# Kernel tuning notes

Measured on AMD Instinct MI355X. Metric: run time of the kernel, lower is better.

## Reference

```python
import jax, jax.numpy as jnp
import numpy as np

N = 100000      # nodes
E = 1600000     # edges (avg degree 16)
F = 64          # input node features
H = 128         # hidden channels
R = 20          # num relations (edge types)
G = 64          # graphs in batch
C = 10          # num classes
L = 2           # num RGCN layers
EPS = 1e-5      # BatchNorm eps


def setup_inputs() -> dict:
    key = jax.random.key(0)
    ks = jax.random.split(key, 14)
    s = 0.05
    return {
        "x": jax.random.normal(ks[0], (N, F), jnp.float32),
        "edge_index": jax.random.randint(ks[1], (2, E), 0, N, jnp.int32),
        "edge_type": jax.random.randint(ks[2], (E,), 0, R, jnp.int32),
        "batch": jnp.sort(jax.random.randint(ks[3], (N,), 0, G, jnp.int32)),
        # params
        "w_in": jax.random.normal(ks[4], (F, H), jnp.float32) * s,
        "b_in": jnp.zeros((H,), jnp.float32),
        "rel_w": jax.random.normal(ks[5], (L, R, H, H), jnp.float32) * s,
        "root_w": jax.random.normal(ks[6], (L, H, H), jnp.float32) * s,
        "conv_b": jnp.zeros((L, H), jnp.float32),
        "bn_g": jnp.ones((L, H), jnp.float32),
        "bn_b": jnp.zeros((L, H), jnp.float32),
        "w_out": jax.random.normal(ks[7], (H, C), jnp.float32) * s,
        "b_out": jnp.zeros((C,), jnp.float32),
    }


def reference(x, edge_index, edge_type, batch, w_in, b_in, rel_w, root_w,
              conv_b, bn_g, bn_b, w_out, b_out):
    # input MLP (dropout is identity in eval)
    h = jax.nn.relu(x @ w_in + b_in)

    src, dst = edge_index[0], edge_index[1]
    # per-(dst,relation) in-degree for RGCNConv mean aggregation
    comb = dst * R + edge_type                             # [E]
    cnt = jax.ops.segment_sum(jnp.ones((E,), jnp.float32), comb,
                              num_segments=N * R)
    edge_norm = (1.0 / jnp.maximum(cnt, 1.0))[comb]        # [E]

    for l in range(L):
        msg = h[src] * edge_norm[:, None]                  # [E, H] normalized source feats
        out = h @ root_w[l] + conv_b[l]                    # root/self transform + bias
        for r in range(R):
            mask = (edge_type == r).astype(h.dtype)        # [E]
            agg = jax.ops.segment_sum(msg * mask[:, None], dst,
                                      num_segments=N)      # [N, H] per-relation mean
            out = out + agg @ rel_w[l, r]
        # BatchNorm1d (training-mode batch statistics over nodes)
        mu = out.mean(axis=0)
        var = out.var(axis=0)
        out = (out - mu) * jax.lax.rsqrt(var + EPS) * bn_g[l] + bn_b[l]
        h = jax.nn.relu(out)                               # dropout = identity (eval)

    # global mean pool over graphs
    sums = jax.ops.segment_sum(h, batch, num_segments=G)   # [G, H]
    counts = jax.ops.segment_sum(jnp.ones((N,), h.dtype), batch, num_segments=G)
    pooled = sums / jnp.maximum(counts, 1.0)[:, None]

    logits = pooled @ w_out + b_out                        # [G, C]
    return jax.nn.sigmoid(logits)
```

## Files before the change

### kernel.cpp

```cpp
#include <hip/hip_runtime.h>

#define N_NODES 100000
#define E_EDGES 1600000
#define F_IN    64
#define H_DIM   128
#define R_REL   20
#define G_GRAPHS 64
#define C_CLASSES 10
#define L_LAYERS 2
#define BN_EPS  1e-5f
#define RN      (R_REL * N_NODES)

typedef unsigned short u16;
typedef unsigned int   u32;
typedef __attribute__((ext_vector_type(8))) short short8;
typedef __attribute__((ext_vector_type(4))) float f32x4;

static __device__ __forceinline__ float bf2f(u16 u) {
    u32 b = ((u32)u) << 16;
    return __builtin_bit_cast(float, b);
}
static __device__ __forceinline__ u16 f2bf(float f) {
    u32 x = __builtin_bit_cast(u32, f);
    u32 r = x + 0x7fff + ((x >> 16) & 1);
    return (u16)(r >> 16);
}


__global__ void count_kernel(const int* __restrict__ ei, const int* __restrict__ et,
                             int* __restrict__ hist) {
    for (int e = blockIdx.x * blockDim.x + threadIdx.x; e < E_EDGES;
         e += gridDim.x * blockDim.x) {
        int t = et[e];
        int d = ei[E_EDGES + e];
        atomicAdd(&hist[t * N_NODES + d], 1);
    }
}

__global__ void scan1_kernel(const int* __restrict__ in, int* __restrict__ out,
                             int* __restrict__ part, int n) {
    __shared__ int s[256];
    int t = threadIdx.x;
    int base = blockIdx.x * 1024;
    int v[4]; int sum = 0;
#pragma unroll
    for (int j = 0; j < 4; ++j) {
        int i = base + t * 4 + j;
        v[j] = (i < n) ? in[i] : 0;
        sum += v[j];
    }
    s[t] = sum;
    __syncthreads();
    for (int off = 1; off < 256; off <<= 1) {
        int x = (t >= off) ? s[t - off] : 0;
        __syncthreads();
        s[t] += x;
        __syncthreads();
    }
    if (t == 255) part[blockIdx.x] = s[255];
    int run = s[t] - sum;
#pragma unroll
    for (int j = 0; j < 4; ++j) {
        int i = base + t * 4 + j;
        if (i < n) out[i] = run;
        run += v[j];
    }
}

__global__ void scan2_kernel(int* __restrict__ part, int nb) {
    __shared__ int s[256];
    int t = threadIdx.x;
    int loc[8]; int sum = 0;
#pragma unroll
    for (int j = 0; j < 8; ++j) {
        int i = t * 8 + j;
        loc[j] = (i < nb) ? part[i] : 0;
        sum += loc[j];
    }
    s[t] = sum;
    __syncthreads();
    for (int off = 1; off < 256; off <<= 1) {
        int x = (t >= off) ? s[t - off] : 0;
        __syncthreads();
        s[t] += x;
        __syncthreads();
    }
    int run = s[t] - sum;
#pragma unroll
    for (int j = 0; j < 8; ++j) {
        int i = t * 8 + j;
        if (i < nb) part[i] = run;
        run += loc[j];
    }
}

__global__ void scan3_kernel(int* __restrict__ out, int* __restrict__ cur2,
                             const int* __restrict__ part, int n) {
    for (int i = blockIdx.x * blockDim.x + threadIdx.x; i < n;
         i += gridDim.x * blockDim.x) {
        int v = out[i] + part[i >> 10];
        out[i] = v;
        cur2[i] = v;
    }
}

__global__ void finalize_kernel(int* __restrict__ off2) {
    if (threadIdx.x == 0) off2[RN] = E_EDGES;
}

__global__ void bucket_kernel(const int* __restrict__ ei, const int* __restrict__ et,
                              int* __restrict__ cur2, int2* __restrict__ epair) {
    for (int e = blockIdx.x * blockDim.x + threadIdx.x; e < E_EDGES;
         e += gridDim.x * blockDim.x) {
        int t = et[e];
        int s = ei[e];
        int d = ei[E_EDGES + e];
        int pos = atomicAdd(&cur2[t * N_NODES + d], 1);
        epair[pos] = make_int2(s, d);
    }
}

template<int K>
__global__ void pack_w(const float* __restrict__ W, u16* __restrict__ Wp) {
    const float* w = W + (size_t)blockIdx.x * K * H_DIM;
    u16* p = Wp + (size_t)blockIdx.x * K * H_DIM;
    for (int o = threadIdx.x; o < K * H_DIM; o += blockDim.x) {
        int j  = o & 7;
        int l  = (o >> 3) & 63;
        int ct = (o >> 9) & 7;
        int kt = o >> 12;
        int k  = kt * 32 + (l >> 4) * 8 + j;
        int n  = ct * 16 + (l & 15);
        p[o] = f2bf(w[(size_t)k * H_DIM + n]);
    }
}

__global__ void cvt_bf16_kernel(const float* __restrict__ in, u16* __restrict__ out, int n4) {
    for (int i = blockIdx.x * blockDim.x + threadIdx.x; i < n4;
         i += gridDim.x * blockDim.x) {
        float4 v = ((const float4*)in)[i];
        ushort4 o;
        o.x = f2bf(v.x); o.y = f2bf(v.y); o.z = f2bf(v.z); o.w = f2bf(v.w);
        ((ushort4*)out)[i] = o;
    }
}

template<int K, bool RELU, bool HASBIAS, bool OUTBF16>
__global__ __launch_bounds__(256)
void mfma_dense(const u16* __restrict__ A, const u16* __restrict__ Wp,
                const float* __restrict__ bias, void* __restrict__ OutV, int M) {
    constexpr int CH = K / 8;
    __shared__ u16 Ws[K * H_DIM];
    __shared__ u16 As[64 * H_DIM];

    for (int o = threadIdx.x; o < K * H_DIM / 8; o += 256)
        ((short8*)Ws)[o] = ((const short8*)Wp)[o];

    const int lane = threadIdx.x & 63;
    const int wave = threadIdx.x >> 6;
    const int l15  = lane & 15;
    const int kgrp = lane >> 4;
    const int arow = wave * 16 + l15;

    for (int tb = blockIdx.x * 64; tb < M; tb += gridDim.x * 64) {
        __syncthreads();
        for (int o = threadIdx.x; o < 64 * CH; o += 256) {
            int row = o / CH, cc = o % CH;
            int grow = tb + row;
            short8 v = {0,0,0,0,0,0,0,0};
            if (grow < M) v = *(const short8*)&A[(size_t)grow * K + cc * 8];
            *(short8*)&As[row * K + ((cc ^ (row & 7)) * 8)] = v;
        }
        __syncthreads();

        f32x4 acc[8];
#pragma unroll
        for (int i = 0; i < 8; ++i) {
            acc[i][0] = 0.f; acc[i][1] = 0.f; acc[i][2] = 0.f; acc[i][3] = 0.f;
        }
#pragma unroll
        for (int kt = 0; kt < K / 32; ++kt) {
            short8 af = *(const short8*)&As[arow * K + (((kt * 4 + kgrp) ^ (arow & 7)) * 8)];
#pragma unroll
            for (int ct = 0; ct < 8; ++ct) {
                short8 bf = *(const short8*)&Ws[(((kt * 8 + ct) * 64) + lane) * 8];
                acc[ct] = __builtin_amdgcn_mfma_f32_16x16x32_bf16(af, bf, acc[ct], 0, 0, 0);
            }
        }

        if (OUTBF16) {
            __syncthreads();
#pragma unroll
            for (int ct = 0; ct < 8; ++ct) {
#pragma unroll
                for (int r = 0; r < 4; ++r) {
                    int row = wave * 16 + kgrp * 4 + r;
                    int col = ct * 16 + l15;
                    float v = acc[ct][r];
                    if (HASBIAS) v += bias[col];
                    if (RELU)    v = fmaxf(v, 0.f);
                    As[row * H_DIM + ((((col >> 3) ^ (row & 7)) << 3) | (col & 7))] = f2bf(v);
                }
            }
            __syncthreads();
            u16* Out = (u16*)OutV;
            for (int o = threadIdx.x; o < 64 * 16; o += 256) {
                int row = o >> 4, cc = o & 15;
                int grow = tb + row;
                if (grow < M)
                    *(short8*)&Out[(size_t)grow * H_DIM + cc * 8] =
                        *(const short8*)&As[row * H_DIM + ((cc ^ (row & 7)) << 3)];
            }
        } else {
            float* Out = (float*)OutV;
#pragma unroll
            for (int ct = 0; ct < 8; ++ct) {
#pragma unroll
                for (int r = 0; r < 4; ++r) {
                    int grow = tb + wave * 16 + kgrp * 4 + r;
                    if (grow < M) {
                        float v = acc[ct][r];
                        if (HASBIAS) v += bias[ct * 16 + l15];
                        if (RELU)    v = fmaxf(v, 0.f);
                        Out[(size_t)grow * H_DIM + ct * 16 + l15] = v;
                    }
                }
            }
        }
    }
}

__global__ __launch_bounds__(256, 4)
void rgcn_conv(const u16* __restrict__ h, const u16* __restrict__ Wrel,
               const u16* __restrict__ Wroot, const float* __restrict__ bias,
               const int2* __restrict__ epair, const int* __restrict__ off2,
               float* __restrict__ outb, float* __restrict__ bn_sums) {
    __shared__ int offs[R_REL][65];
    __shared__ u16 Abf[64 * H_DIM];
    __shared__ float bnS[H_DIM], bnSS[H_DIM];

    const int d0 = blockIdx.x * 64;
    for (int i = threadIdx.x; i < R_REL * 65; i += 256) {
        int r = i / 65, j = i % 65;
        offs[r][j] = off2[r * N_NODES + min(d0 + j, N_NODES)];
    }
    if (threadIdx.x < H_DIM) { bnS[threadIdx.x] = 0.f; bnSS[threadIdx.x] = 0.f; }

    const int lane = threadIdx.x & 63;
    const int wv   = threadIdx.x >> 6;
    const int l15  = lane & 15;
    const int kgrp = lane >> 4;
    const int arow = wv * 16 + l15;
    const u32* h2  = (const u32*)h;
    u32* Ab32 = (u32*)Abf;

    f32x4 acc[8];
#pragma unroll
    for (int i = 0; i < 8; ++i) {
        acc[i][0] = 0.f; acc[i][1] = 0.f; acc[i][2] = 0.f; acc[i][3] = 0.f;
    }

    auto flushrow = [&](int dcur, int cnt, float f0, float f1) {
        float nm = 1.0f / (float)cnt;
        int dr = dcur - d0;
        u32 pk = (u32)f2bf(f0 * nm) | ((u32)f2bf(f1 * nm) << 16);
        Ab32[dr * 64 + ((((lane >> 2) ^ (dr & 7)) << 2) | (lane & 3))] = pk;
    };

    __syncthreads();

    for (int r = 0; r < R_REL; ++r) {
        const int estart = __builtin_amdgcn_readfirstlane(offs[r][wv * 16]);
        const int eend   = __builtin_amdgcn_readfirstlane(offs[r][wv * 16 + 16]);
        if (eend <= estart) continue;

#pragma unroll
        for (int i = 0; i < 16; ++i)
            Ab32[(wv * 16 + i) * 64 + lane] = 0u;

        {
            const int last = eend - 1;
            int ss[16], dd[16];
            u32 rv[16];
#pragma unroll
            for (int j = 0; j < 16; ++j) {
                int2 pr = epair[min(estart + j, last)];
                ss[j] = pr.x; dd[j] = pr.y;
            }
#pragma unroll
            for (int j = 0; j < 16; ++j)
                rv[j] = h2[(size_t)ss[j] * 64 + lane];

            int dcur = -1, cnt = 0;
            float f0 = 0.f, f1 = 0.f;
#pragma unroll
            for (int j = 0; j < 16; ++j) {
                if (estart + j < eend) {
                    if (dd[j] != dcur) {
                        if (dcur >= 0) flushrow(dcur, cnt, f0, f1);
                        dcur = dd[j]; f0 = 0.f; f1 = 0.f; cnt = 0;
                    }
                    f0 += bf2f((u16)(rv[j] & 0xffff));
                    f1 += bf2f((u16)(rv[j] >> 16));
                    cnt++;
                }
            }
            for (int e = estart + 16; e < eend; e += 16) {
                int ss2[16], dd2[16];
                u32 rv2[16];
#pragma unroll
                for (int j = 0; j < 16; ++j) {
                    int2 pr = epair[min(e + j, last)];
                    ss2[j] = pr.x; dd2[j] = pr.y;
                }
#pragma unroll
                for (int j = 0; j < 16; ++j)
                    rv2[j] = h2[(size_t)ss2[j] * 64 + lane];
#pragma unroll
                for (int j = 0; j < 16; ++j) {
                    if (e + j < eend) {
                        if (dd2[j] != dcur) {
                            if (dcur >= 0) flushrow(dcur, cnt, f0, f1);
                            dcur = dd2[j]; f0 = 0.f; f1 = 0.f; cnt = 0;
                        }
                        f0 += bf2f((u16)(rv2[j] & 0xffff));
                        f1 += bf2f((u16)(rv2[j] >> 16));
                        cnt++;
                    }
                }
            }
            if (dcur >= 0) flushrow(dcur, cnt, f0, f1);
        }

        const u16* Wr = Wrel + (size_t)r * H_DIM * H_DIM;
#pragma unroll
        for (int kt = 0; kt < 4; ++kt) {
            short8 af = *(const short8*)&Abf[arow * H_DIM + (((kt * 4 + kgrp) ^ (arow & 7)) * 8)];
#pragma unroll
            for (int ct = 0; ct < 8; ++ct) {
                short8 bf = *(const short8*)&Wr[(((kt * 8 + ct) * 64) + lane) * 8];
                acc[ct] = __builtin_amdgcn_mfma_f32_16x16x32_bf16(af, bf, acc[ct], 0, 0, 0);
            }
        }
    }

    {
        const int hrow = min(d0 + arow, N_NODES - 1);
#pragma unroll
        for (int kt = 0; kt < 4; ++kt) {
            short8 af = *(const short8*)&h[(size_t)hrow * H_DIM + kt * 32 + kgrp * 8];
#pragma unroll
            for (int ct = 0; ct < 8; ++ct) {
                short8 bf = *(const short8*)&Wroot[(((kt * 8 + ct) * 64) + lane) * 8];
                acc[ct] = __builtin_amdgcn_mfma_f32_16x16x32_bf16(af, bf, acc[ct], 0, 0, 0);
            }
        }
    }

#pragma unroll
    for (int ct = 0; ct < 8; ++ct) {
        float bv = bias[ct * 16 + l15];
        float sl = 0.f, sq = 0.f;
#pragma unroll
        for (int rr = 0; rr < 4; ++rr) {
            int grow = d0 + wv * 16 + kgrp * 4 + rr;
            if (grow < N_NODES) {
                float v = acc[ct][rr] + bv;
                outb[(size_t)grow * H_DIM + ct * 16 + l15] = v;
                sl += v;
                sq += v * v;
            }
        }
        sl += __shfl_xor(sl, 16); sl += __shfl_xor(sl, 32);
        sq += __shfl_xor(sq, 16); sq += __shfl_xor(sq, 32);
        if (kgrp == 0) {
            atomicAdd(&bnS[ct * 16 + l15], sl);
            atomicAdd(&bnSS[ct * 16 + l15], sq);
        }
    }
    __syncthreads();
    if (threadIdx.x < H_DIM) {
        atomicAdd(&bn_sums[threadIdx.x], bnS[threadIdx.x]);
        atomicAdd(&bn_sums[H_DIM + threadIdx.x], bnSS[threadIdx.x]);
    }
}

__global__ void bn_apply(const float* __restrict__ X, const float* __restrict__ sums,
                         const float* __restrict__ gg, const float* __restrict__ bb,
                         u16* __restrict__ Hout) {
    __shared__ float sc[H_DIM], sh[H_DIM];
    if (threadIdx.x < H_DIM) {
        float mean = sums[threadIdx.x] * (1.0f / N_NODES);
        float var  = sums[H_DIM + threadIdx.x] * (1.0f / N_NODES) - mean * mean;
        float inv  = rsqrtf(var + BN_EPS) * gg[threadIdx.x];
        sc[threadIdx.x] = inv;
        sh[threadIdx.x] = bb[threadIdx.x] - mean * inv;
    }
    __syncthreads();
    int total = N_NODES * (H_DIM / 4);
    for (int idx = blockIdx.x * 256 + threadIdx.x; idx < total; idx += gridDim.x * 256) {
        float4 v = ((const float4*)X)[idx];
        int c = (idx & 31) << 2;
        ushort4 o;
        o.x = f2bf(fmaxf(v.x * sc[c + 0] + sh[c + 0], 0.f));
        o.y = f2bf(fmaxf(v.y * sc[c + 1] + sh[c + 1], 0.f));
        o.z = f2bf(fmaxf(v.z * sc[c + 2] + sh[c + 2], 0.f));
        o.w = f2bf(fmaxf(v.w * sc[c + 3] + sh[c + 3], 0.f));
        ((ushort4*)Hout)[idx] = o;
    }
}

__global__ void pool_kernel(const u16* __restrict__ Hf, const int* __restrict__ batch,
                            float* __restrict__ pool, float* __restrict__ pcnt) {
    int col  = threadIdx.x & 127;
    int half = threadIdx.x >> 7;
    int chunk = (N_NODES + gridDim.x - 1) / gridDim.x;
    int start = blockIdx.x * chunk;
    int end   = min(N_NODES, start + chunk);
    int curg = -1;
    float acc = 0.f, c = 0.f;
    for (int row = start + half; row < end; row += 2) {
        int g = batch[row];
        if (g != curg) {
            if (curg >= 0) {
                atomicAdd(&pool[curg * H_DIM + col], acc);
                if (col == 0) atomicAdd(&pcnt[curg], c);
            }
            curg = g; acc = 0.f; c = 0.f;
        }
        acc += bf2f(Hf[(size_t)row * H_DIM + col]);
        c += 1.f;
    }
    if (curg >= 0) {
        atomicAdd(&pool[curg * H_DIM + col], acc);
        if (col == 0) atomicAdd(&pcnt[curg], c);
    }
}

__global__ void logits_kernel(const float* __restrict__ pool, const float* __restrict__ pcnt,
                              const float* __restrict__ w_out, const float* __restrict__ b_out,
                              float* __restrict__ out) {
    int g = blockIdx.x;
    __shared__ float p[H_DIM];
    float cnt = fmaxf(pcnt[g], 1.0f);
    p[threadIdx.x] = pool[g * H_DIM + threadIdx.x] / cnt;
    __syncthreads();
    if (threadIdx.x < C_CLASSES) {
        float acc = b_out[threadIdx.x];
        for (int k = 0; k < H_DIM; ++k)
            acc += p[k] * w_out[k * C_CLASSES + threadIdx.x];
        out[g * C_CLASSES + threadIdx.x] = 1.0f / (1.0f + expf(-acc));
    }
}

static inline size_t align256(size_t x) { return (x + 255) & ~(size_t)255; }

extern "C" void kernel_launch(void* const* d_in, const int* in_sizes, int n_in,
                              void* d_out, int out_size, void* d_ws, size_t ws_size,
                              hipStream_t stream) {
    const float* x      = (const float*)d_in[0];
    const int*   ei     = (const int*)d_in[1];
    const int*   et     = (const int*)d_in[2];
    const int*   batch  = (const int*)d_in[3];
    const float* w_in   = (const float*)d_in[4];
    const float* b_in   = (const float*)d_in[5];
    const float* rel_w  = (const float*)d_in[6];
    const float* root_w = (const float*)d_in[7];
    const float* conv_b = (const float*)d_in[8];
    const float* bn_g   = (const float*)d_in[9];
    const float* bn_b   = (const float*)d_in[10];
    const float* w_out  = (const float*)d_in[11];
    const float* b_out  = (const float*)d_in[12];
    float* out = (float*)d_out;

    char* ws = (char*)d_ws;
    size_t off = 0;
    u16*   h_bf  = (u16*)(ws + off);  off += align256((size_t)N_NODES * H_DIM * 2);
    float* outb  = (float*)(ws + off); off += align256((size_t)N_NODES * H_DIM * 4);
    u16*   x_bf  = (u16*)(ws + off);  off += align256((size_t)N_NODES * F_IN * 2);
    int*   off2  = (int*)(ws + off);  off += align256((size_t)(RN + 1) * 4 + 256);
    int*   cur2  = (int*)(ws + off);  off += align256((size_t)RN * 4);
    int2*  e_pair = (int2*)(ws + off); off += align256((size_t)E_EDGES * 8 + 256);
    u16*   wp_in   = (u16*)(ws + off); off += align256((size_t)F_IN * H_DIM * 2);
    u16*   wp_root = (u16*)(ws + off); off += align256((size_t)L_LAYERS * H_DIM * H_DIM * 2);
    u16*   wp_rel  = (u16*)(ws + off); off += align256((size_t)L_LAYERS * R_REL * H_DIM * H_DIM * 2);
    int*   scan_part  = (int*)(ws + off); off += align256(2048 * 4);
    float* bn_sums    = (float*)(ws + off); off += align256(2 * H_DIM * 4);
    float* pool       = (float*)(ws + off); off += align256((size_t)G_GRAPHS * H_DIM * 4);
    float* pcnt       = (float*)(ws + off); off += 256;

    hipMemsetAsync(cur2, 0, (size_t)RN * 4, stream);
    count_kernel<<<1024, 256, 0, stream>>>(ei, et, cur2);
    const int NB = (RN + 1023) / 1024;
    scan1_kernel<<<NB, 256, 0, stream>>>(cur2, off2, scan_part, RN);
    scan2_kernel<<<1, 256, 0, stream>>>(scan_part, NB);
    scan3_kernel<<<2048, 256, 0, stream>>>(off2, cur2, scan_part, RN);
    finalize_kernel<<<1, 64, 0, stream>>>(off2);
    bucket_kernel<<<2048, 256, 0, stream>>>(ei, et, cur2, e_pair);

    cvt_bf16_kernel<<<2048, 256, 0, stream>>>(x, x_bf, N_NODES * F_IN / 4);
    pack_w<F_IN><<<1, 256, 0, stream>>>(w_in, wp_in);
    pack_w<H_DIM><<<L_LAYERS, 256, 0, stream>>>(root_w, wp_root);
    pack_w<H_DIM><<<L_LAYERS * R_REL, 256, 0, stream>>>(rel_w, wp_rel);

    mfma_dense<F_IN, true, true, true><<<dim3(640), 256, 0, stream>>>(
        x_bf, wp_in, b_in, h_bf, N_NODES);

    const int CONV_BLOCKS = (N_NODES + 63) / 64;
    for (int l = 0; l < L_LAYERS; ++l) {
        hipMemsetAsync(bn_sums, 0, 2 * H_DIM * 4, stream);
        rgcn_conv<<<dim3(CONV_BLOCKS), 256, 0, stream>>>(
            h_bf, wp_rel + (size_t)l * R_REL * H_DIM * H_DIM,
            wp_root + (size_t)l * H_DIM * H_DIM, conv_b + (size_t)l * H_DIM,
            e_pair, off2, outb, bn_sums);
        bn_apply<<<2048, 256, 0, stream>>>(outb, bn_sums,
                                           bn_g + (size_t)l * H_DIM,
                                           bn_b + (size_t)l * H_DIM, h_bf);
    }

    hipMemsetAsync(pool, 0, (size_t)G_GRAPHS * H_DIM * 4, stream);
    hipMemsetAsync(pcnt, 0, 256, stream);
    pool_kernel<<<512, 256, 0, stream>>>(h_bf, batch, pool, pcnt);
    logits_kernel<<<G_GRAPHS, 128, 0, stream>>>(pool, pcnt, w_out, b_out, out);
}
```

Before: 817.6 us.

## Process 32 destination rows per wave to reuse weight fragments across two MFMA tiles

Each block of the RGCN conv kernel now covers 128 destination nodes instead of 64, with each wave owning 32 rows split into two 16-row MFMA subtiles. Relation and root weight fragments are loaded once per k-step and reused for both subtiles, halving the weight-load traffic per output row. The cost is doubled accumulator registers, which drops occupancy (launch bounds 4 to 3), and a larger LDS tile. Per-relation edge ranges per wave also get longer, so there are fewer kernel blocks with more serial gather work each.

```diff
diff --git a/kernel.cpp b/kernel.cpp
--- a/kernel.cpp
+++ b/kernel.cpp
@@ -230,19 +230,19 @@
     }
 }
 
-__global__ __launch_bounds__(256, 4)
+__global__ __launch_bounds__(256, 3)
 void rgcn_conv(const u16* __restrict__ h, const u16* __restrict__ Wrel,
                const u16* __restrict__ Wroot, const float* __restrict__ bias,
                const int2* __restrict__ epair, const int* __restrict__ off2,
                float* __restrict__ outb, float* __restrict__ bn_sums) {
-    __shared__ int offs[R_REL][65];
-    __shared__ u16 Abf[64 * H_DIM];
+    __shared__ int offsB[R_REL][5];
+    __shared__ u16 Abf[128 * H_DIM];
     __shared__ float bnS[H_DIM], bnSS[H_DIM];
 
-    const int d0 = blockIdx.x * 64;
-    for (int i = threadIdx.x; i < R_REL * 65; i += 256) {
-        int r = i / 65, j = i % 65;
-        offs[r][j] = off2[r * N_NODES + min(d0 + j, N_NODES)];
+    const int d0 = blockIdx.x * 128;
+    for (int i = threadIdx.x; i < R_REL * 5; i += 256) {
+        int r = i / 5, j = i % 5;
+        offsB[r][j] = off2[r * N_NODES + min(d0 + j * 32, N_NODES)];
     }
     if (threadIdx.x < H_DIM) { bnS[threadIdx.x] = 0.f; bnSS[threadIdx.x] = 0.f; }
 
@@ -250,15 +250,18 @@
     const int wv   = threadIdx.x >> 6;
     const int l15  = lane & 15;
     const int kgrp = lane >> 4;
-    const int arow = wv * 16 + l15;
+    const int rbase = wv * 32;
     const u32* h2  = (const u32*)h;
     u32* Ab32 = (u32*)Abf;
 
-    f32x4 acc[8];
-#pragma unroll
-    for (int i = 0; i < 8; ++i) {
-        acc[i][0] = 0.f; acc[i][1] = 0.f; acc[i][2] = 0.f; acc[i][3] = 0.f;
-    }
+    f32x4 acc[2][8];
+#pragma unroll
+    for (int s = 0; s < 2; ++s)
+#pragma unroll
+        for (int i = 0; i < 8; ++i) {
+            acc[s][i][0] = 0.f; acc[s][i][1] = 0.f;
+            acc[s][i][2] = 0.f; acc[s][i][3] = 0.f;
+        }
 
     auto flushrow = [&](int dcur, int cnt, float f0, float f1) {
         float nm = 1.0f / (float)cnt;
@@ -270,61 +273,38 @@
     __syncthreads();
 
     for (int r = 0; r < R_REL; ++r) {
-        const int estart = __builtin_amdgcn_readfirstlane(offs[r][wv * 16]);
-        const int eend   = __builtin_amdgcn_readfirstlane(offs[r][wv * 16 + 16]);
+        const int estart = __builtin_amdgcn_readfirstlane(offsB[r][wv]);
+        const int eend   = __builtin_amdgcn_readfirstlane(offsB[r][wv + 1]);
         if (eend <= estart) continue;
 
 #pragma unroll
-        for (int i = 0; i < 16; ++i)
-            Ab32[(wv * 16 + i) * 64 + lane] = 0u;
+        for (int i = 0; i < 32; ++i)
+            Ab32[(rbase + i) * 64 + lane] = 0u;
 
         {
             const int last = eend - 1;
-            int ss[16], dd[16];
-            u32 rv[16];
-#pragma unroll
-            for (int j = 0; j < 16; ++j) {
-                int2 pr = epair[min(estart + j, last)];
-                ss[j] = pr.x; dd[j] = pr.y;
-            }
-#pragma unroll
-            for (int j = 0; j < 16; ++j)
-                rv[j] = h2[(size_t)ss[j] * 64 + lane];
-
             int dcur = -1, cnt = 0;
             float f0 = 0.f, f1 = 0.f;
-#pragma unroll
-            for (int j = 0; j < 16; ++j) {
-                if (estart + j < eend) {
-                    if (dd[j] != dcur) {
-                        if (dcur >= 0) flushrow(dcur, cnt, f0, f1);
-                        dcur = dd[j]; f0 = 0.f; f1 = 0.f; cnt = 0;
-                    }
-                    f0 += bf2f((u16)(rv[j] & 0xffff));
-                    f1 += bf2f((u16)(rv[j] >> 16));
-                    cnt++;
-                }
-            }
-            for (int e = estart + 16; e < eend; e += 16) {
-                int ss2[16], dd2[16];
-                u32 rv2[16];
+            for (int e = estart; e < eend; e += 16) {
+                int ss[16], dd[16];
+                u32 rv[16];
 #pragma unroll
                 for (int j = 0; j < 16; ++j) {
                     int2 pr = epair[min(e + j, last)];
-                    ss2[j] = pr.x; dd2[j] = pr.y;
+                    ss[j] = pr.x; dd[j] = pr.y;
                 }
 #pragma unroll
                 for (int j = 0; j < 16; ++j)
-                    rv2[j] = h2[(size_t)ss2[j] * 64 + lane];
+                    rv[j] = h2[(size_t)ss[j] * 64 + lane];
 #pragma unroll
                 for (int j = 0; j < 16; ++j) {
                     if (e + j < eend) {
-                        if (dd2[j] != dcur) {
+                        if (dd[j] != dcur) {
                             if (dcur >= 0) flushrow(dcur, cnt, f0, f1);
-                            dcur = dd2[j]; f0 = 0.f; f1 = 0.f; cnt = 0;
+                            dcur = dd[j]; f0 = 0.f; f1 = 0.f; cnt = 0;
                         }
-                        f0 += bf2f((u16)(rv2[j] & 0xffff));
-                        f1 += bf2f((u16)(rv2[j] >> 16));
+                        f0 += bf2f((u16)(rv[j] & 0xffff));
+                        f1 += bf2f((u16)(rv[j] >> 16));
                         cnt++;
                     }
                 }
@@ -335,47 +315,59 @@
         const u16* Wr = Wrel + (size_t)r * H_DIM * H_DIM;
 #pragma unroll
         for (int kt = 0; kt < 4; ++kt) {
-            short8 af = *(const short8*)&Abf[arow * H_DIM + (((kt * 4 + kgrp) ^ (arow & 7)) * 8)];
-#pragma unroll
-            for (int ct = 0; ct < 8; ++ct) {
-                short8 bf = *(const short8*)&Wr[(((kt * 8 + ct) * 64) + lane) * 8];
-                acc[ct] = __builtin_amdgcn_mfma_f32_16x16x32_bf16(af, bf, acc[ct], 0, 0, 0);
-            }
-        }
-    }
-
-    {
-        const int hrow = min(d0 + arow, N_NODES - 1);
-#pragma unroll
-        for (int kt = 0; kt < 4; ++kt) {
+            short8 bf[8];
+#pragma unroll
+            for (int ct = 0; ct < 8; ++ct)
+                bf[ct] = *(const short8*)&Wr[(((kt * 8 + ct) * 64) + lane) * 8];
+#pragma unroll
+            for (int s = 0; s < 2; ++s) {
+                const int arow = rbase + s * 16 + l15;
+                short8 af = *(const short8*)&Abf[arow * H_DIM + (((kt * 4 + kgrp) ^ (arow & 7)) * 8)];
+#pragma unroll
+                for (int ct = 0; ct < 8; ++ct)
+                    acc[s][ct] = __builtin_amdgcn_mfma_f32_16x16x32_bf16(af, bf[ct], acc[s][ct], 0, 0, 0);
+            }
+        }
+    }
+
+#pragma unroll
+    for (int kt = 0; kt < 4; ++kt) {
+        short8 bf[8];
+#pragma unroll
+        for (int ct = 0; ct < 8; ++ct)
+            bf[ct] = *(const short8*)&Wroot[(((kt * 8 + ct) * 64) + lane) * 8];
+#pragma unroll
+        for (int s = 0; s < 2; ++s) {
+            const int hrow = min(d0 + rbase + s * 16 + l15, N_NODES - 1);
             short8 af = *(const short8*)&h[(size_t)hrow * H_DIM + kt * 32 + kgrp * 8];
 #pragma unroll
-            for (int ct = 0; ct < 8; ++ct) {
-                short8 bf = *(const short8*)&Wroot[(((kt * 8 + ct) * 64) + lane) * 8];
-                acc[ct] = __builtin_amdgcn_mfma_f32_16x16x32_bf16(af, bf, acc[ct], 0, 0, 0);
-            }
-        }
-    }
-
-#pragma unroll
-    for (int ct = 0; ct < 8; ++ct) {
-        float bv = bias[ct * 16 + l15];
-        float sl = 0.f, sq = 0.f;
-#pragma unroll
-        for (int rr = 0; rr < 4; ++rr) {
-            int grow = d0 + wv * 16 + kgrp * 4 + rr;
-            if (grow < N_NODES) {
-                float v = acc[ct][rr] + bv;
-                outb[(size_t)grow * H_DIM + ct * 16 + l15] = v;
-                sl += v;
-                sq += v * v;
-            }
-        }
-        sl += __shfl_xor(sl, 16); sl += __shfl_xor(sl, 32);
-        sq += __shfl_xor(sq, 16); sq += __shfl_xor(sq, 32);
-        if (kgrp == 0) {
-            atomicAdd(&bnS[ct * 16 + l15], sl);
-            atomicAdd(&bnSS[ct * 16 + l15], sq);
+            for (int ct = 0; ct < 8; ++ct)
+                acc[s][ct] = __builtin_amdgcn_mfma_f32_16x16x32_bf16(af, bf[ct], acc[s][ct], 0, 0, 0);
+        }
+    }
+
+#pragma unroll
+    for (int s = 0; s < 2; ++s) {
+#pragma unroll
+        for (int ct = 0; ct < 8; ++ct) {
+            float bv = bias[ct * 16 + l15];
+            float sl = 0.f, sq = 0.f;
+#pragma unroll
+            for (int rr = 0; rr < 4; ++rr) {
+                int grow = d0 + rbase + s * 16 + kgrp * 4 + rr;
+                if (grow < N_NODES) {
+                    float v = acc[s][ct][rr] + bv;
+                    outb[(size_t)grow * H_DIM + ct * 16 + l15] = v;
+                    sl += v;
+                    sq += v * v;
+                }
+            }
+            sl += __shfl_xor(sl, 16); sl += __shfl_xor(sl, 32);
+            sq += __shfl_xor(sq, 16); sq += __shfl_xor(sq, 32);
+            if (kgrp == 0) {
+                atomicAdd(&bnS[ct * 16 + l15], sl);
+                atomicAdd(&bnSS[ct * 16 + l15], sq);
+            }
         }
     }
     __syncthreads();
@@ -506,7 +498,7 @@
     mfma_dense<F_IN, true, true, true><<<dim3(640), 256, 0, stream>>>(
         x_bf, wp_in, b_in, h_bf, N_NODES);
 
-    const int CONV_BLOCKS = (N_NODES + 63) / 64;
+    const int CONV_BLOCKS = (N_NODES + 127) / 128;
     for (int l = 0; l < L_LAYERS; ++l) {
         hipMemsetAsync(bn_sums, 0, 2 * H_DIM * 4, stream);
         rgcn_conv<<<dim3(CONV_BLOCKS), 256, 0, stream>>>(
```

Result: no change. 828.4 us (+1.3%).
